# Kernel optimization log

Hardware: AMD Instinct MI355X
Metric: run time of the kernel (lower is better)

## Reference

```python
import jax, jax.numpy as jnp
import numpy as np

K = 15  # PSF kernel size


def conv3(x, w, b):
    # 3x3 conv, stride 1, padding 1, NCHW/OIHW
    y = jax.lax.conv_general_dilated(x, w, (1, 1), ((1, 1), (1, 1)),
                                     dimension_numbers=("NCHW", "OIHW", "NCHW"))
    return y + b[None, :, None, None]


def setup_inputs() -> dict:
    key = jax.random.key(0)
    ks = jax.random.split(key, 22)
    S = 0.05  # small init scale to keep activations / softmax logits sane
    p = lambda k, shape: (jax.random.normal(k, shape, jnp.float32) * S)
    return {
        "raw_image": jax.random.uniform(ks[0], (1, 4, 256, 256), jnp.float32),
        "aberration_features": jax.random.normal(ks[1], (1, 128, 256, 256), jnp.float32),
        # psf_predictor: 128->256->128->4*225
        "pw1": p(ks[2], (256, 128, 3, 3)), "pb1": p(ks[3], (256,)),
        "pw2": p(ks[4], (128, 256, 3, 3)), "pb2": p(ks[5], (128,)),
        "pw3": p(ks[6], (900, 128, 3, 3)), "pb3": p(ks[7], (900,)),
        # freq_corrector: 8->64->64->8
        "fw1": p(ks[8], (64, 8, 3, 3)),  "fb1": p(ks[9], (64,)),
        "fw2": p(ks[10], (64, 64, 3, 3)), "fb2": p(ks[11], (64,)),
        "fw3": p(ks[12], (8, 64, 3, 3)),  "fb3": p(ks[13], (8,)),
        # per-channel correctors (4 of them), stacked on leading dim: 1->16->16->1
        "cw1": p(ks[14], (4, 16, 1, 3, 3)),  "cb1": p(ks[15], (4, 16)),
        "cw2": p(ks[16], (4, 16, 16, 3, 3)), "cb2": p(ks[17], (4, 16)),
        "cw3": p(ks[18], (4, 1, 16, 3, 3)),  "cb3": p(ks[19], (4, 1)),
    }


def reference(raw_image, aberration_features,
              pw1, pb1, pw2, pb2, pw3, pb3,
              fw1, fb1, fw2, fb2, fw3, fb3,
              cw1, cb1, cw2, cb2, cw3, cb3):
    B, C, H, W = raw_image.shape
    # --- PSF prediction ---
    h = jax.nn.relu(conv3(aberration_features, pw1, pb1))
    h = jax.nn.relu(conv3(h, pw2, pb2))
    psf = conv3(h, pw3, pb3).reshape(B, C, K * K, H, W)
    psf = jax.nn.softmax(psf, axis=2)  # normalize over the K*K taps
    # --- spatially-varying deconv: unfold + weighted reduce ---
    pad = K // 2
    xp = jnp.pad(raw_image, ((0, 0), (0, 0), (pad, pad), (pad, pad)), mode="reflect")
    patches = jax.lax.conv_general_dilated_patches(
        xp, (K, K), (1, 1), "VALID", dimension_numbers=("NCHW", "OIHW", "NCHW"))
    patches = patches.reshape(B, C, K * K, H, W)  # channel-major like F.unfold
    corrected = jnp.sum(patches * psf, axis=2)  # [B,C,H,W]
    # --- frequency-domain correction ---
    fft = jnp.fft.rfft2(corrected, norm="ortho")  # [B,C,H,W//2+1] complex
    fri = jnp.concatenate([fft.real, fft.imag], axis=1)  # [B,2C,...]
    g = jax.nn.relu(conv3(fri, fw1, fb1))
    g = jax.nn.relu(conv3(g, fw2, fb2))
    g = conv3(g, fw3, fb3)
    cf = jax.lax.complex(g[:, :C], g[:, C:])
    corrected = corrected + jnp.fft.irfft2(cf, s=(H, W), norm="ortho")
    # --- per-channel refinement (4 small distinct conv stacks) ---
    outs = []
    for i in range(C):
        ch = corrected[:, i:i + 1]
        ch = jax.nn.relu(conv3(ch, cw1[i], cb1[i]))
        ch = jax.nn.relu(conv3(ch, cw2[i], cb2[i]))
        ch = conv3(ch, cw3[i], cb3[i])
        outs.append(ch)
    corrected = jnp.concatenate(outs, axis=1)
    return jnp.clip(raw_image + corrected, 0.0, 1.0)
```

## Files before the change

### kernel.cpp

```cpp
#include <hip/hip_runtime.h>
#include <hip/hip_bf16.h>
#include <math.h>

#define PI_F 3.14159265358979323846f
#define PERM4(s) ((((s)&3)) + 8*(((s)>>2)&1) + 4*((s)>>3))

typedef short bfrag __attribute__((ext_vector_type(8)));
typedef float f32x4 __attribute__((ext_vector_type(4)));
typedef float f32x16 __attribute__((ext_vector_type(16)));
typedef unsigned short us8 __attribute__((ext_vector_type(8)));

__device__ inline unsigned bf16rne(float x) {
    unsigned u = __builtin_bit_cast(unsigned, x);
    return (u + 0x7fffu + ((u >> 16) & 1u)) >> 16;
}
__device__ inline unsigned packbf2(float a, float b) {
    return bf16rne(a) | (bf16rne(b) << 16);
}
__device__ inline float bf2f(unsigned short u) {
    return __builtin_bit_cast(float, (unsigned)u << 16);
}
__device__ inline void glds16(const unsigned short* g, unsigned char* l) {
    __builtin_amdgcn_global_load_lds(
        (const __attribute__((address_space(1))) unsigned int*)g,
        (__attribute__((address_space(3))) unsigned int*)l, 16, 0, 0);
}

template<bool RELU, int CT, bool SM>
__global__ __launch_bounds__(256, (CT == 2) ? 4 : 5) void conv_v9(
    const unsigned short* __restrict__ inb, const short* __restrict__ wp,
    const float* __restrict__ bias, unsigned short* __restrict__ ob,
    int C32, int Cout, int COT, int CBmax,
    const float* __restrict__ rawc, float* __restrict__ corr)
{
    int bid = blockIdx.x;
    bid = (bid & 7) * 128 + (bid >> 3);
    const int y  = bid >> 2;
    const int x0 = (bid & 3) << 6;
    const int t  = threadIdx.x;
    const int l  = t & 63;
    const int col = l & 31, kh = l >> 5;
    const int wv = t >> 6;
    const int ctg0 = wv * CT;

    __shared__ __align__(16) unsigned char sB[2][13824];

    f32x16 acc[CT][2];
#pragma unroll
    for (int ct = 0; ct < CT; ++ct)
#pragma unroll
        for (int n = 0; n < 2; ++n)
#pragma unroll
            for (int i = 0; i < 16; ++i) acc[ct][n][i] = 0.f;

    int ba3[3];
#pragma unroll
    for (int dx = 0; dx < 3; ++dx) {
        int px = col + 3 + dx;
        ba3[dx] = px * 64 + ((kh ^ ((px >> 1) & 3)) << 4);
    }

    int srcoff[4];
    bool vmask[4];
#pragma unroll
    for (int i = 0; i < 4; ++i) {
        int q = i * 256 + t;
        bool qv = q < 864;
        int row = q / 288;  if (row > 2) row = 2;
        int qr = q - row * 288;
        int px = qr >> 2, j = qr & 3;
        int u = j ^ ((px >> 1) & 3);
        int gx = x0 - 4 + px;
        int gy = y - 1 + row;
        vmask[i] = qv && ((unsigned)gx < 256u) && ((unsigned)gy < 256u);
        srcoff[i] = (((u >> 1) * 256 + gy) * 256 + gx) * 16 + (u & 1) * 8;
    }

    auto STAGE = [&](int c32, unsigned char* bufb) {
        const int coff = c32 * 2097152;
#pragma unroll
        for (int i = 0; i < 4; ++i)
            if (vmask[i])
                glds16(inb + (srcoff[i] + coff), bufb + (i << 12) + (wv << 10));
    };

    for (int i = t; i < 1728; i += 256)
        *(uint4*)(&sB[0][0] + i * 16) = make_uint4(0, 0, 0, 0);
    __syncthreads();

    const bfrag* wA = (const bfrag*)wp;
    const int tstr = C32 * 2 * COT * 64;

    auto LOAD_AF = [&](bfrag (&af)[3][CT], int abase, int dy) {
#pragma unroll
        for (int dx = 0; dx < 3; ++dx)
#pragma unroll
            for (int ct = 0; ct < CT; ++ct)
                af[dx][ct] = wA[abase + ct * 64 + (size_t)(dy * 3 + dx) * tstr];
    };
    auto MFMA_DY = [&](const bfrag (&af)[3][CT], const unsigned char* rp, int csx) {
#pragma unroll
        for (int dx = 0; dx < 3; ++dx) {
            const int ba = ba3[dx] ^ csx;
            bfrag b0 = *(const bfrag*)(rp + ba);
            bfrag b1 = *(const bfrag*)(rp + ba + 2048);
#pragma unroll
            for (int ct = 0; ct < CT; ++ct) {
                acc[ct][0] = __builtin_amdgcn_mfma_f32_32x32x16_bf16(af[dx][ct], b0, acc[ct][0], 0, 0, 0);
                acc[ct][1] = __builtin_amdgcn_mfma_f32_32x32x16_bf16(af[dx][ct], b1, acc[ct][1], 0, 0, 0);
            }
        }
    };

    STAGE(0, sB[0]);
    __syncthreads();
    for (int c32 = 0; c32 < C32; ++c32) {
        const unsigned char* bufp = sB[c32 & 1];
        const int ab0 = (c32 * 2 * COT + ctg0) * 64 + l;
        const int ab1 = ((c32 * 2 + 1) * COT + ctg0) * 64 + l;
        bfrag af0[3][CT];
        LOAD_AF(af0, ab0, 0);
        if (c32 + 1 < C32) STAGE(c32 + 1, sB[(c32 + 1) & 1]);
        MFMA_DY(af0, bufp, 0);
#pragma unroll
        for (int dy = 1; dy < 3; ++dy) {
            bfrag af[3][CT];
            LOAD_AF(af, ab0, dy);
            MFMA_DY(af, bufp + dy * 4608, 0);
        }
#pragma unroll
        for (int dy = 0; dy < 3; ++dy) {
            bfrag af[3][CT];
            LOAD_AF(af, ab1, dy);
            MFMA_DY(af, bufp + dy * 4608, 32);
        }
        __syncthreads();
    }

    if (SM) {
        float* sRaw  = (float*)&sB[0][0];
        float* sBias = (float*)&sB[0][4800];
        int*   sOff  = (int*)&sB[0][5700];
        float* red   = (float*)&sB[1][0];
        for (int i = t; i < 1200; i += 256) {
            int r = i / 80, xx = i - r * 80;
            int gy = y + r - 7;
            gy = gy < 0 ? -gy : (gy > 255 ? 510 - gy : gy);
            int gx = x0 + xx - 7;
            gx = gx < 0 ? -gx : (gx > 255 ? 510 - gx : gx);
            sRaw[i] = rawc[gy * 256 + gx];
        }
        if (t < 225) {
            sBias[t] = bias[t];
            sOff[t]  = t + 65 * (t / 15);
        }
        __syncthreads();

        float pm[2], ps[2], pa[2];
#pragma unroll
        for (int n = 0; n < 2; ++n) {
            float m = -1e30f, s = 0.f, a = 0.f;
            const int xb = col + n * 32;
#pragma unroll
            for (int ct = 0; ct < CT; ++ct) {
                const f32x16 A = acc[ct][n];
#pragma unroll
                for (int rh = 0; rh < 2; ++rh) {
                    int cb = (ctg0 + ct) * 2 + rh;
#pragma unroll
                    for (int j = 0; j < 8; ++j) {
                        int co = cb * 16 + (j & 3) + 8 * (j >> 2) + 4 * kh;
                        if (co < 225) {
                            float lv = A[rh * 8 + j] + sBias[co];
                            float pv = sRaw[sOff[co] + xb];
                            if (lv > m + 4.f) { float rs = __expf(m - lv); s *= rs; a *= rs; m = lv; }
                            float e = __expf(lv - m);
                            s += e; a += e * pv;
                        }
                    }
                }
            }
            float mo = __shfl_xor(m, 32), so = __shfl_xor(s, 32), ao = __shfl_xor(a, 32);
            float M = fmaxf(m, mo);
            float e0 = __expf(m - M), e1 = __expf(mo - M);
            pm[n] = M;
            ps[n] = s * e0 + so * e1;
            pa[n] = a * e0 + ao * e1;
        }
        if (kh == 0) {
#pragma unroll
            for (int n = 0; n < 2; ++n) {
                int px = col + n * 32;
                red[(px * 4 + wv) * 3 + 0] = pm[n];
                red[(px * 4 + wv) * 3 + 1] = ps[n];
                red[(px * 4 + wv) * 3 + 2] = pa[n];
            }
        }
        __syncthreads();
        if (t < 64) {
            float m = red[(t * 4) * 3], s = red[(t * 4) * 3 + 1], a = red[(t * 4) * 3 + 2];
#pragma unroll
            for (int gg = 1; gg < 4; ++gg) {
                float mg = red[(t * 4 + gg) * 3], sg = red[(t * 4 + gg) * 3 + 1], ag = red[(t * 4 + gg) * 3 + 2];
                float M = fmaxf(m, mg);
                float s0 = __expf(m - M), s1 = __expf(mg - M);
                s = s * s0 + sg * s1;
                a = a * s0 + ag * s1;
                m = M;
            }
            corr[y * 256 + x0 + t] = a / s;
        }
    } else {
#pragma unroll
        for (int ct = 0; ct < CT; ++ct) {
            const int ctg = ctg0 + ct;
#pragma unroll
            for (int n = 0; n < 2; ++n) {
                const int xx = x0 + col + n * 32;
                const f32x16 A = acc[ct][n];
#pragma unroll
                for (int rh = 0; rh < 2; ++rh) {
                    int cb = ctg * 2 + rh;
                    if (cb >= CBmax) continue;
                    unsigned wd[4];
#pragma unroll
                    for (int jp = 0; jp < 4; ++jp) {
                        float vv[2];
#pragma unroll
                        for (int e = 0; e < 2; ++e) {
                            int j = jp * 2 + e;
                            int co = cb * 16 + (j & 3) + 8 * (j >> 2) + 4 * kh;
                            float bv = (co < Cout) ? bias[co] : 0.f;
                            float v = A[rh * 8 + j] + bv;
                            if (RELU) v = fmaxf(v, 0.f);
                            vv[e] = v;
                        }
                        wd[jp] = packbf2(vv[0], vv[1]);
                    }
                    *(uint4*)(ob + ((((size_t)cb << 8) + y) * 256 + xx) * 16 + (kh << 3)) =
                        make_uint4(wd[0], wd[1], wd[2], wd[3]);
                }
            }
        }
    }
}

template<bool RELU, bool OUT_BF16, int CT>
__global__ __launch_bounds__(256, 3) void conv_v4(
    const unsigned short* __restrict__ inb, const short* __restrict__ wp,
    const float* __restrict__ bias, void* __restrict__ outv,
    int C32, int Cout, int COT, int W, int RSg, int CBmax)
{
    const int tilesx = (W + 127) >> 7;
    const int y  = blockIdx.x / tilesx;
    const int x0 = (blockIdx.x % tilesx) << 7;
    const int t  = threadIdx.x;
    const int l  = t & 63;
    const int col = l & 31, kh = l >> 5;
    const int wv = t >> 6;
    const int wct = wv & 1, wpt = wv >> 1;
    const int ctg0 = (blockIdx.y * 2 + wct) * CT;

    __shared__ __align__(16) unsigned char sB[26112];

    f32x16 acc[CT][2];
#pragma unroll
    for (int ct = 0; ct < CT; ++ct)
#pragma unroll
        for (int n = 0; n < 2; ++n)
#pragma unroll
            for (int i = 0; i < 16; ++i) acc[ct][n][i] = 0.f;

    int ba3[3];
#pragma unroll
    for (int dx = 0; dx < 3; ++dx) {
        int px = wpt * 64 + col + 3 + dx;
        ba3[dx] = px * 64 + ((kh ^ ((px >> 1) & 3)) << 4);
    }

    const int pxm = (t & 127) + 4, thalf = t >> 7;
    const int gxm = x0 + (t & 127);
    const bool gxok = gxm < W;
    const int offm_e = pxm * 64 + ((thalf ^ ((pxm >> 1) & 3)) << 4);
    const int hr = t >> 5, hj = t & 31, hg = hj >> 3, hp = hj & 7;
    const int hslot = hp + ((hp >> 2) << 7);
    const int hgx = x0 - 4 + hslot;
    const int hoff = hr * 8704 + hslot * 64 + ((hg ^ ((hslot >> 1) & 3)) << 4);
    const int hgy = y + hr - 1;
    const bool hok = (t < 96) && ((unsigned)hgy < 256u) && ((unsigned)hgx < (unsigned)W);

    auto STAGE = [&](int c32) {
        const int cb0 = c32 << 1;
#pragma unroll
        for (int k = 0; k < 6; ++k) {
            const int r = k >> 1;
            const int cb = cb0 + (k & 1);
            const int gy = y + r - 1;
            uint4 v = make_uint4(0, 0, 0, 0);
            if (gxok && (unsigned)gy < 256u)
                v = *(const uint4*)(inb + ((((size_t)cb << 8) + gy) * RSg + gxm) * 16 + (thalf << 3));
            *(uint4*)(sB + r * 8704 + (offm_e ^ ((k & 1) << 5))) = v;
        }
        if (t < 96) {
            uint4 v = make_uint4(0, 0, 0, 0);
            if (hok) v = *(const uint4*)(inb + ((((size_t)(cb0 + (hg >> 1)) << 8) + hgy) * RSg + hgx) * 16 + ((hg & 1) << 3));
            *(uint4*)(sB + hoff) = v;
        }
    };

    const bfrag* wA = (const bfrag*)wp;
    const int tstr = C32 * 2 * COT * 64;

    STAGE(0);
    __syncthreads();
    for (int c32 = 0; c32 < C32; ++c32) {
#pragma unroll 1
        for (int cs = 0; cs < 2; ++cs) {
            const int abase = ((c32 * 2 + cs) * COT + ctg0) * 64 + l;
            const int csx = cs << 5;
#pragma unroll
            for (int dy = 0; dy < 3; ++dy) {
                bfrag af[3][CT];
#pragma unroll
                for (int dx = 0; dx < 3; ++dx)
#pragma unroll
                    for (int ct = 0; ct < CT; ++ct)
                        af[dx][ct] = wA[abase + ct * 64 + (size_t)(dy * 3 + dx) * tstr];
                const unsigned char* rp = sB + dy * 8704;
#pragma unroll
                for (int dx = 0; dx < 3; ++dx) {
                    const int ba = ba3[dx] ^ csx;
                    bfrag b0 = *(const bfrag*)(rp + ba);
                    bfrag b1 = *(const bfrag*)(rp + ba + 2048);
#pragma unroll
                    for (int ct = 0; ct < CT; ++ct) {
                        acc[ct][0] = __builtin_amdgcn_mfma_f32_32x32x16_bf16(af[dx][ct], b0, acc[ct][0], 0, 0, 0);
                        acc[ct][1] = __builtin_amdgcn_mfma_f32_32x32x16_bf16(af[dx][ct], b1, acc[ct][1], 0, 0, 0);
                    }
                }
            }
        }
        __syncthreads();
        if (c32 + 1 < C32) { STAGE(c32 + 1); __syncthreads(); }
    }

    const int xBase = x0 + wpt * 64 + col;
#pragma unroll
    for (int ct = 0; ct < CT; ++ct) {
        const int ctg = ctg0 + ct;
#pragma unroll
        for (int n = 0; n < 2; ++n) {
            int xx = xBase + n * 32;
            if (xx >= W) continue;
            const f32x16 A = acc[ct][n];
            if (OUT_BF16) {
                unsigned short* ob = (unsigned short*)outv;
#pragma unroll
                for (int rh = 0; rh < 2; ++rh) {
                    int cb = ctg * 2 + rh;
                    if (cb >= CBmax) continue;
                    unsigned wd[4];
#pragma unroll
                    for (int jp = 0; jp < 4; ++jp) {
                        float vv[2];
#pragma unroll
                        for (int e = 0; e < 2; ++e) {
                            int j = jp * 2 + e;
                            int co = cb * 16 + (j & 3) + 8 * (j >> 2) + 4 * kh;
                            float bv = (co < Cout) ? bias[co] : 0.f;
                            float v = A[rh * 8 + j] + bv;
                            if (RELU) v = fmaxf(v, 0.f);
                            vv[e] = v;
                        }
                        wd[jp] = packbf2(vv[0], vv[1]);
                    }
                    *(uint4*)(ob + ((((size_t)cb << 8) + y) * RSg + xx) * 16 + (kh << 3)) =
                        make_uint4(wd[0], wd[1], wd[2], wd[3]);
                }
            } else {
                float* of = (float*)outv;
#pragma unroll
                for (int reg = 0; reg < 16; ++reg) {
                    int co = ctg * 32 + (reg & 3) + 8 * (reg >> 2) + 4 * kh;
                    if (co < Cout) {
                        float v = A[reg] + bias[co];
                        if (RELU) v = fmaxf(v, 0.f);
                        of[(((size_t)co << 8) + y) * RSg + xx] = v;
                    }
                }
            }
        }
    }
}

__global__ __launch_bounds__(256) void repack_wA(
    const float* __restrict__ w, unsigned short* __restrict__ o,
    int Cin, int C32, int Cout, int COT)
{
    int total = 9 * C32 * 2 * COT * 512;
    for (int i = blockIdx.x * 256 + threadIdx.x; i < total; i += gridDim.x * 256) {
        int j = i & 7;
        int l = (i >> 3) & 63;
        int rest = i >> 9;
        int ct = rest % COT; rest /= COT;
        int cs = rest & 1; rest >>= 1;
        int c32 = rest % C32;
        int tap = rest / C32;
        int co = ct * 32 + (l & 31);
        int s = ((l >> 5) << 3) + j;
        int ci = c32 * 32 + cs * 16 + PERM4(s);
        float v = (co < Cout && ci < Cin) ? w[((size_t)co * Cin + ci) * 9 + tap] : 0.f;
        o[i] = (unsigned short)bf16rne(v);
    }
}

__global__ __launch_bounds__(256) void cvt_blocked(
    const float* __restrict__ src, unsigned short* __restrict__ dst, int C)
{
    int cb = blockIdx.x >> 8;
    int y  = blockIdx.x & 255;
    int x  = threadIdx.x;
    unsigned wd[8];
#pragma unroll
    for (int q = 0; q < 8; ++q) {
        float v[2];
#pragma unroll
        for (int e = 0; e < 2; ++e) {
            int s = q * 2 + e;
            int ci = (cb << 4) + PERM4(s);
            v[e] = (ci < C) ? src[((size_t)ci * 256 + y) * 256 + x] : 0.f;
        }
        wd[q] = packbf2(v[0], v[1]);
    }
    unsigned short* dp = dst + (((size_t)cb << 16) + (y << 8) + x) * 16;
    *(uint4*)dp = make_uint4(wd[0], wd[1], wd[2], wd[3]);
    *(uint4*)(dp + 8) = make_uint4(wd[4], wd[5], wd[6], wd[7]);
}

__global__ __launch_bounds__(256) void repack_wr2(
    const float* __restrict__ cw2, unsigned short* __restrict__ o)
{
    int i = blockIdx.x * 256 + threadIdx.x;
    if (i >= 10240) return;
    int k = i & 31, rest = i >> 5;
    int co = rest & 15;
    int kt = (rest >> 4) % 5;
    int ch = rest / 80;
    int tap = 2 * kt + (k >= 16 ? 1 : 0), ci = k & 15;
    float v = 0.f;
    if (tap < 9) v = cw2[(((size_t)ch * 16 + co) * 16 + ci) * 9 + tap];
    o[i] = (unsigned short)bf16rne(v);
}

__global__ __launch_bounds__(256) void refine1_kernel(
    const float* __restrict__ corrected, const float* __restrict__ cw1,
    const float* __restrict__ cb1, unsigned short* __restrict__ h1b)
{
    const int c = blockIdx.x >> 8;
    const int y = blockIdx.x & 255;
    const int t = threadIdx.x;
    __shared__ float sIn[3][258];
    __shared__ float sW[144];
    __shared__ float sBv[16];
    if (t < 144) sW[t] = cw1[c * 144 + t];
    if (t >= 144 && t < 160) sBv[t - 144] = cb1[c * 16 + (t - 144)];
    for (int i = t; i < 774; i += 256) {
        int r = i / 258, xx = i % 258;
        int gy = y + r - 1, gx = xx - 1;
        sIn[r][xx] = ((unsigned)gy < 256u && (unsigned)gx < 256u)
                   ? corrected[((size_t)c * 256 + gy) * 256 + gx] : 0.f;
    }
    __syncthreads();
    float a[9];
#pragma unroll
    for (int dy = 0; dy < 3; ++dy)
#pragma unroll
        for (int dx = 0; dx < 3; ++dx) a[dy * 3 + dx] = sIn[dy][t + dx];
    unsigned short ov[16];
#pragma unroll
    for (int co = 0; co < 16; ++co) {
        float acc = sBv[co];
#pragma unroll
        for (int tap = 0; tap < 9; ++tap) acc += a[tap] * sW[co * 9 + tap];
        acc = fmaxf(acc, 0.f);
        ov[co] = (unsigned short)bf16rne(acc);
    }
    unsigned short* op = h1b + ((((size_t)c * 256 + y) * 256 + t) << 4);
    *(uint4*)op = *(uint4*)ov;
    *(uint4*)(op + 8) = *(uint4*)(ov + 8);
}

__global__ __launch_bounds__(256) void refine2_mfma(
    const unsigned short* __restrict__ h1b, const unsigned short* __restrict__ wr2,
    const float* __restrict__ cb2, unsigned short* __restrict__ h2b)
{
    const int c = blockIdx.x >> 8;
    const int y = blockIdx.x & 255;
    const int t = threadIdx.x;
    const int l15 = t & 15, lg = (t >> 4) & 3, wv = t >> 6;

    __shared__ __align__(16) unsigned char sA[3 * 258 * 32];

    for (int i = t; i < 1548; i += 256) {
        int r = i / 516, u = i % 516;
        int px = u >> 1, half = u & 1;
        int gy = y + r - 1, gx = px - 1;
        uint4 v = make_uint4(0, 0, 0, 0);
        if ((unsigned)gy < 256u && (unsigned)gx < 256u)
            v = *(const uint4*)(h1b + ((((size_t)c * 256 + gy) * 256 + gx) << 4) + (half << 3));
        *(uint4*)(sA + r * 8256 + px * 32 + ((half ^ ((px >> 2) & 1)) << 4)) = v;
    }
    __syncthreads();

    f32x4 acc[4];
#pragma unroll
    for (int n = 0; n < 4; ++n) acc[n] = (f32x4){0.f, 0.f, 0.f, 0.f};
    const bfrag* wf = (const bfrag*)(wr2 + (size_t)c * 2560);
    const int strip = wv * 64;
#pragma unroll
    for (int kt = 0; kt < 5; ++kt) {
        bfrag a = wf[(kt * 16 + l15) * 4 + lg];
        int tap1 = 2 * kt + 1; if (tap1 > 8) tap1 = 8;
        int tap = (lg < 2) ? (2 * kt) : tap1;
        int dy = tap / 3, dx = tap % 3;
#pragma unroll
        for (int n = 0; n < 4; ++n) {
            int pxs = strip + n * 16 + l15 + dx;
            bfrag b = *(const bfrag*)(sA + dy * 8256 + pxs * 32 +
                                      (((lg & 1) ^ ((pxs >> 2) & 1)) << 4));
            acc[n] = __builtin_amdgcn_mfma_f32_16x16x32_bf16(a, b, acc[n], 0, 0, 0);
        }
    }

#pragma unroll
    for (int n = 0; n < 4; ++n) {
        int px = strip + n * 16 + l15;
        unsigned short ov[4];
#pragma unroll
        for (int r = 0; r < 4; ++r) {
            int co = lg * 4 + r;
            float v = acc[n][r] + cb2[c * 16 + co];
            v = fmaxf(v, 0.f);
            ov[r] = (unsigned short)bf16rne(v);
        }
        *(ushort4*)(h2b + ((((size_t)c * 256 + y) * 256 + px) << 4) + lg * 4) = *(ushort4*)ov;
    }
}

__global__ __launch_bounds__(256) void refine3_kernel(
    const unsigned short* __restrict__ h2b, const float* __restrict__ cw3,
    const float* __restrict__ cb3, const float* __restrict__ raw,
    float* __restrict__ out)
{
    const int c = blockIdx.x >> 8;
    const int y = blockIdx.x & 255;
    const int t = threadIdx.x;
    __shared__ __align__(16) unsigned char sA[3 * 258 * 32];
    __shared__ float sW[144];
    if (t < 144) sW[t] = cw3[c * 144 + t];
    for (int i = t; i < 1548; i += 256) {
        int r = i / 516, u = i % 516;
        int px = u >> 1, half = u & 1;
        int gy = y + r - 1, gx = px - 1;
        uint4 v = make_uint4(0, 0, 0, 0);
        if ((unsigned)gy < 256u && (unsigned)gx < 256u)
            v = *(const uint4*)(h2b + ((((size_t)c * 256 + gy) * 256 + gx) << 4) + (half << 3));
        *(uint4*)(sA + r * 8256 + px * 32 + ((half ^ ((px >> 2) & 1)) << 4)) = v;
    }
    __syncthreads();
    float acc = cb3[c];
#pragma unroll
    for (int tap = 0; tap < 9; ++tap) {
        int dy = tap / 3, dx = tap % 3;
        int px = t + dx;
        const unsigned char* p = sA + dy * 8256 + px * 32;
        int sw = ((px >> 2) & 1) << 4;
        us8 h0 = *(const us8*)(p + (sw ^ 0));
        us8 h1 = *(const us8*)(p + (sw ^ 16));
#pragma unroll
        for (int j = 0; j < 8; ++j) acc += bf2f(h0[j]) * sW[j * 9 + tap];
#pragma unroll
        for (int j = 0; j < 8; ++j) acc += bf2f(h1[j]) * sW[(8 + j) * 9 + tap];
    }
    size_t idx = ((size_t)c * 256 + y) * 256 + t;
    float v = raw[idx] + acc;
    out[idx] = fminf(fmaxf(v, 0.f), 1.f);
}

__global__ __launch_bounds__(256) void rdft_row_kernel(
    const float* __restrict__ x, float2* __restrict__ z)
{
    int cy = blockIdx.x;
    __shared__ float row[256];
    __shared__ float ct[256], st[256];
    int t = threadIdx.x;
    row[t] = x[cy * 256 + t];
    float a = (2.0f * PI_F / 256.0f) * (float)t;
    ct[t] = cosf(a);
    st[t] = sinf(a);
    __syncthreads();
    if (t < 129) {
        float re = 0.f, im = 0.f;
        int idx = 0;
        for (int n = 0; n < 256; ++n) {
            float v = row[n];
            re += v * ct[idx];
            im -= v * st[idx];
            idx = (idx + t) & 255;
        }
        z[cy * 129 + t] = make_float2(re, im);
    }
}

__global__ __launch_bounds__(256) void dft_col_fwd2(
    const float2* __restrict__ z, unsigned short* __restrict__ fri16)
{
    int c  = blockIdx.x >> 8;
    int k1 = blockIdx.x & 255;
    __shared__ float ct[256], st[256];
    int t = threadIdx.x;
    float a = (2.0f * PI_F / 256.0f) * (float)t;
    ct[t] = cosf(a);
    st[t] = sinf(a);
    __syncthreads();
    if (t < 129) {
        float re = 0.f, im = 0.f;
        int idx = 0;
        for (int n1 = 0; n1 < 256; ++n1) {
            float2 zv = z[(c * 256 + n1) * 129 + t];
            float cw = ct[idx], sw = st[idx];
            re += zv.x * cw + zv.y * sw;
            im += zv.y * cw - zv.x * sw;
            idx = (idx + k1) & 255;
        }
        const float sc = 1.0f / 256.0f;
        size_t base = ((size_t)k1 * 132 + t) * 16;
        fri16[base + c]     = (unsigned short)bf16rne(re * sc);
        fri16[base + 8 + c] = (unsigned short)bf16rne(im * sc);
    }
}

__global__ __launch_bounds__(256) void dft_col_inv_kernel(
    const float* __restrict__ g, float2* __restrict__ z)
{
    int c  = blockIdx.x >> 8;
    int n1 = blockIdx.x & 255;
    __shared__ float ct[256], st[256];
    int t = threadIdx.x;
    float a = (2.0f * PI_F / 256.0f) * (float)t;
    ct[t] = cosf(a);
    st[t] = sinf(a);
    __syncthreads();
    if (t < 129) {
        float re = 0.f, im = 0.f;
        int idx = 0;
        for (int k1 = 0; k1 < 256; ++k1) {
            float gr = g[((size_t)c * 256 + k1) * 132 + t];
            float gi = g[((size_t)(4 + c) * 256 + k1) * 132 + t];
            float cw = ct[idx], sw = st[idx];
            re += gr * cw - gi * sw;
            im += gi * cw + gr * sw;
            idx = (idx + n1) & 255;
        }
        z[(c * 256 + n1) * 129 + t] = make_float2(re, im);
    }
}

__global__ __launch_bounds__(256) void irdft_row_add_kernel(
    const float2* __restrict__ z, float* __restrict__ corrected)
{
    int c  = blockIdx.x >> 8;
    int n1 = blockIdx.x & 255;
    __shared__ float2 yrow[129];
    __shared__ float ct[256], st[256];
    int t = threadIdx.x;
    if (t < 129) yrow[t] = z[(c * 256 + n1) * 129 + t];
    float a = (2.0f * PI_F / 256.0f) * (float)t;
    ct[t] = cosf(a);
    st[t] = sinf(a);
    __syncthreads();
    float acc = yrow[0].x + ((t & 1) ? -yrow[128].x : yrow[128].x);
    int idx = t;
    for (int k = 1; k <= 127; ++k) {
        float2 yv = yrow[k];
        acc += 2.0f * (yv.x * ct[idx] - yv.y * st[idx]);
        idx = (idx + t) & 255;
    }
    corrected[c * 65536 + n1 * 256 + t] += acc * (1.0f / 256.0f);
}

extern "C" void kernel_launch(void* const* d_in, const int* in_sizes, int n_in,
                              void* d_out, int out_size, void* d_ws, size_t ws_size,
                              hipStream_t stream)
{
    const float* raw = (const float*)d_in[0];
    const float* ab  = (const float*)d_in[1];
    const float* pw1 = (const float*)d_in[2];  const float* pb1 = (const float*)d_in[3];
    const float* pw2 = (const float*)d_in[4];  const float* pb2 = (const float*)d_in[5];
    const float* pw3 = (const float*)d_in[6];  const float* pb3 = (const float*)d_in[7];
    const float* fw1 = (const float*)d_in[8];  const float* fb1 = (const float*)d_in[9];
    const float* fw2 = (const float*)d_in[10]; const float* fb2 = (const float*)d_in[11];
    const float* fw3 = (const float*)d_in[12]; const float* fb3 = (const float*)d_in[13];
    const float* cw1 = (const float*)d_in[14]; const float* cb1 = (const float*)d_in[15];
    const float* cw2 = (const float*)d_in[16]; const float* cb2 = (const float*)d_in[17];
    const float* cw3 = (const float*)d_in[18]; const float* cb3 = (const float*)d_in[19];
    float* out = (float*)d_out;

    char* B = (char*)d_ws;
    unsigned short* h1b     = (unsigned short*)(B);
    unsigned short* h2b     = (unsigned short*)(B + 33554432);
    unsigned short* h1r     = (unsigned short*)(B + 33554432);
    unsigned short* h2r     = (unsigned short*)(B + 41943040);
    float* corrected = (float*)(B + 50331648);
    float2* zbuf     = (float2*)(B + 51380224);
    unsigned short* fri16 = (unsigned short*)(B + 53493760);
    unsigned short* g1b   = (unsigned short*)(B + 55656448);
    unsigned short* g2b   = (unsigned short*)(B + 59981824);
    float* gf        = (float*)(B + 64307200);
    unsigned short* rw1  = (unsigned short*)(B + 65388544);
    unsigned short* rw2  = (unsigned short*)(B + 65978368);
    unsigned short* rw3  = (unsigned short*)(B + 66568192);
    unsigned short* rwf1 = (unsigned short*)(B + 68927488);
    unsigned short* rwf2 = (unsigned short*)(B + 68964352);
    unsigned short* rwf3 = (unsigned short*)(B + 69038080);
    unsigned short* wr2r = (unsigned short*)(B + 69111808);
    unsigned short* ab16 = (unsigned short*)(B + 69132288);

    dim3 blk(256);

    repack_wA<<<512, blk, 0, stream>>>(pw1, rw1, 128, 4, 256, 8);
    repack_wA<<<512, blk, 0, stream>>>(pw2, rw2, 256, 8, 128, 4);
    for (int c = 0; c < 4; ++c)
        repack_wA<<<512, blk, 0, stream>>>(
            pw3 + (size_t)c * 225 * 128 * 9, rw3 + (size_t)c * 294912, 128, 4, 225, 8);
    repack_wA<<<64, blk, 0, stream>>>(fw1, rwf1, 8, 1, 64, 2);
    repack_wA<<<128, blk, 0, stream>>>(fw2, rwf2, 64, 2, 64, 2);
    repack_wA<<<128, blk, 0, stream>>>(fw3, rwf3, 64, 2, 8, 2);
    repack_wr2<<<40, blk, 0, stream>>>(cw2, wr2r);
    cvt_blocked<<<2048, blk, 0, stream>>>(ab, ab16, 128);

    conv_v9<true, 2, false><<<1024, blk, 0, stream>>>(
        ab16, (const short*)rw1, pb1, h1b, 4, 256, 8, 16, nullptr, nullptr);
    conv_v9<true, 1, false><<<1024, blk, 0, stream>>>(
        h1b, (const short*)rw2, pb2, h2b, 8, 128, 4, 8, nullptr, nullptr);
    for (int c = 0; c < 4; ++c) {
        conv_v9<false, 2, true><<<1024, blk, 0, stream>>>(
            h2b, (const short*)(rw3 + (size_t)c * 294912), pb3 + c * 225, h1b,
            4, 225, 8, 15, raw + c * 65536, corrected + c * 65536);
    }
    rdft_row_kernel<<<1024, blk, 0, stream>>>(corrected, zbuf);
    hipMemsetAsync(fri16, 0, 2162688, stream);
    dft_col_fwd2<<<1024, blk, 0, stream>>>(zbuf, fri16);
    conv_v4<true, true, 1><<<dim3(512, 1), blk, 0, stream>>>(
        fri16, (const short*)rwf1, fb1, g1b, 1, 64, 2, 129, 132, 4);
    conv_v4<true, true, 1><<<dim3(512, 1), blk, 0, stream>>>(
        g1b, (const short*)rwf2, fb2, g2b, 2, 64, 2, 129, 132, 4);
    conv_v4<false, false, 1><<<dim3(512, 1), blk, 0, stream>>>(
        g2b, (const short*)rwf3, fb3, gf, 2, 8, 2, 129, 132, 0);
    dft_col_inv_kernel<<<1024, blk, 0, stream>>>(gf, zbuf);
    irdft_row_add_kernel<<<1024, blk, 0, stream>>>(zbuf, corrected);
    refine1_kernel<<<1024, blk, 0, stream>>>(corrected, cw1, cb1, h1r);
    refine2_mfma<<<1024, blk, 0, stream>>>(h1r, wr2r, cb2, h2r);
    refine3_kernel<<<1024, blk, 0, stream>>>(h2r, cw3, cb3, raw, out);
}
```

Measured before the change: 472.1 us.

## Batch weight repacks into one launch, skip interior LDS zeroing, raise MFMA priority

Result: faster. 458.2 us (-2.9%).

```diff
diff --git a/kernel.cpp b/kernel.cpp
--- a/kernel.cpp
+++ b/kernel.cpp
@@ -84,9 +84,11 @@
                 glds16(inb + (srcoff[i] + coff), bufb + (i << 12) + (wv << 10));
     };
 
-    for (int i = t; i < 1728; i += 256)
-        *(uint4*)(&sB[0][0] + i * 16) = make_uint4(0, 0, 0, 0);
-    __syncthreads();
+    if (x0 == 0 || x0 == 192 || y == 0 || y == 255) {
+        for (int i = t; i < 1728; i += 256)
+            *(uint4*)(&sB[0][0] + i * 16) = make_uint4(0, 0, 0, 0);
+        __syncthreads();
+    }
 
     const bfrag* wA = (const bfrag*)wp;
     const int tstr = C32 * 2 * COT * 64;
@@ -99,6 +101,7 @@
                 af[dx][ct] = wA[abase + ct * 64 + (size_t)(dy * 3 + dx) * tstr];
     };
     auto MFMA_DY = [&](const bfrag (&af)[3][CT], const unsigned char* rp, int csx) {
+        __builtin_amdgcn_s_setprio(1);
 #pragma unroll
         for (int dx = 0; dx < 3; ++dx) {
             const int ba = ba3[dx] ^ csx;
@@ -110,6 +113,7 @@
                 acc[ct][1] = __builtin_amdgcn_mfma_f32_32x32x16_bf16(af[dx][ct], b1, acc[ct][1], 0, 0, 0);
             }
         }
+        __builtin_amdgcn_s_setprio(0);
     };
 
     STAGE(0, sB[0]);
@@ -393,24 +397,31 @@
     }
 }
 
-__global__ __launch_bounds__(256) void repack_wA(
-    const float* __restrict__ w, unsigned short* __restrict__ o,
-    int Cin, int C32, int Cout, int COT)
-{
-    int total = 9 * C32 * 2 * COT * 512;
-    for (int i = blockIdx.x * 256 + threadIdx.x; i < total; i += gridDim.x * 256) {
+struct RepackJob { const float* w; unsigned short* o; int Cin, C32, Cout, COT, blk0, nblk; };
+struct RepackJobs { RepackJob j[9]; };
+
+__global__ __launch_bounds__(256) void repack_multi(RepackJobs J)
+{
+    int b = blockIdx.x;
+    int ji = 0;
+#pragma unroll
+    for (int k = 1; k < 9; ++k) if (b >= J.j[k].blk0) ji = k;
+    const RepackJob jb = J.j[ji];
+    int rb = b - jb.blk0;
+    int total = 9 * jb.C32 * 2 * jb.COT * 512;
+    for (int i = rb * 256 + threadIdx.x; i < total; i += jb.nblk * 256) {
         int j = i & 7;
         int l = (i >> 3) & 63;
         int rest = i >> 9;
-        int ct = rest % COT; rest /= COT;
+        int ct = rest % jb.COT; rest /= jb.COT;
         int cs = rest & 1; rest >>= 1;
-        int c32 = rest % C32;
-        int tap = rest / C32;
+        int c32 = rest % jb.C32;
+        int tap = rest / jb.C32;
         int co = ct * 32 + (l & 31);
         int s = ((l >> 5) << 3) + j;
         int ci = c32 * 32 + cs * 16 + PERM4(s);
-        float v = (co < Cout && ci < Cin) ? w[((size_t)co * Cin + ci) * 9 + tap] : 0.f;
-        o[i] = (unsigned short)bf16rne(v);
+        float v = (co < jb.Cout && ci < jb.Cin) ? jb.w[((size_t)co * jb.Cin + ci) * 9 + tap] : 0.f;
+        jb.o[i] = (unsigned short)bf16rne(v);
     }
 }
 
@@ -728,14 +739,17 @@
 
     dim3 blk(256);
 
-    repack_wA<<<512, blk, 0, stream>>>(pw1, rw1, 128, 4, 256, 8);
-    repack_wA<<<512, blk, 0, stream>>>(pw2, rw2, 256, 8, 128, 4);
-    for (int c = 0; c < 4; ++c)
-        repack_wA<<<512, blk, 0, stream>>>(
-            pw3 + (size_t)c * 225 * 128 * 9, rw3 + (size_t)c * 294912, 128, 4, 225, 8);
-    repack_wA<<<64, blk, 0, stream>>>(fw1, rwf1, 8, 1, 64, 2);
-    repack_wA<<<128, blk, 0, stream>>>(fw2, rwf2, 64, 2, 64, 2);
-    repack_wA<<<128, blk, 0, stream>>>(fw3, rwf3, 64, 2, 8, 2);
+    RepackJobs J;
+    J.j[0] = { pw1,                    rw1,                128, 4, 256, 8,    0, 512 };
+    J.j[1] = { pw2,                    rw2,                256, 8, 128, 4,  512, 512 };
+    J.j[2] = { pw3 + 0 * 259200,       rw3 + 0 * 294912,   128, 4, 225, 8, 1024, 512 };
+    J.j[3] = { pw3 + 1 * 259200,       rw3 + 1 * 294912,   128, 4, 225, 8, 1536, 512 };
+    J.j[4] = { pw3 + 2 * 259200,       rw3 + 2 * 294912,   128, 4, 225, 8, 2048, 512 };
+    J.j[5] = { pw3 + 3 * 259200,       rw3 + 3 * 294912,   128, 4, 225, 8, 2560, 512 };
+    J.j[6] = { fw1,                    rwf1,                 8, 1,  64, 2, 3072,  64 };
+    J.j[7] = { fw2,                    rwf2,                64, 2,  64, 2, 3136, 128 };
+    J.j[8] = { fw3,                    rwf3,                64, 2,   8, 2, 3264, 128 };
+    repack_multi<<<3392, blk, 0, stream>>>(J);
     repack_wr2<<<40, blk, 0, stream>>>(cw2, wr2r);
     cvt_blocked<<<2048, blk, 0, stream>>>(ab, ab16, 128);
 
```
